# Kernel optimization log

Hardware: AMD Instinct MI355X
Metric: run time of the kernel (lower is better)

## Reference

```python
import jax, jax.numpy as jnp
import numpy as np

NEG_SLOPE = 0.01  # torch.nn.LeakyReLU default


def setup_inputs() -> dict:
    key = jax.random.key(0)
    k1, k2, k3 = jax.random.split(key, 3)
    B, T, U, H, O = 8, 300, 80, 512, 640
    input_TN = jax.random.normal(k1, (B, T, 1, H), dtype=jnp.float32)
    input_PN = jax.random.normal(k2, (B, 1, U, H), dtype=jnp.float32)
    # joint_network: Linear(input_size=2H, n_neurons=O)
    W = jax.random.normal(k3, (2 * H, O), dtype=jnp.float32) / np.sqrt(2 * H)
    b = jnp.zeros((O,), dtype=jnp.float32)
    return {"input_TN": input_TN, "input_PN": input_PN, "W": W, "b": b}


def reference(input_TN, input_PN, W, b):
    # joint == "concat": expand TN/PN to (B,T,U,H), concat on last dim -> (B,T,U,2H),
    # then Linear, then LeakyReLU. Mathematically, Linear(cat(x, y)) ==
    # x @ W[:H] + y @ W[H:] + b, which avoids materializing the (B,T,U,2H) tensor.
    H = input_TN.shape[-1]
    Wt, Wp = W[:H], W[H:]
    tn_proj = jnp.einsum("btuh,ho->btuo", input_TN, Wt)  # (B,T,1,O)
    pn_proj = jnp.einsum("btuh,ho->btuo", input_PN, Wp)  # (B,1,U,O)
    joint = tn_proj + pn_proj + b                         # (B,T,U,O)
    return jax.nn.leaky_relu(joint, negative_slope=NEG_SLOPE)
```

## Files before the change

kernel.cpp:

```cpp
#include <hip/hip_runtime.h>


#define DIM_H 512
#define DIM_O 640
#define DIM_B 8
#define DIM_T 300
#define DIM_U 80
#define M_TN  2400
#define M_PN  640
#define NEG_SLOPE 0.01f

#define BK 32
#define NB_N (DIM_O / 64)
#define NB_TN (((M_TN + 63) / 64) * NB_N)
#define NB_PN (((M_PN + 63) / 64) * NB_N)

typedef float f32x4 __attribute__((ext_vector_type(4)));

__global__ __launch_bounds__(256, 2) void proj_gemm(
    const float* __restrict__ tn_in,
    const float* __restrict__ pn_in,
    const float* __restrict__ W,
    const float* __restrict__ bias,
    float* __restrict__ tn_out,
    float* __restrict__ pn_out)
{
    const int bid = blockIdx.x;
    const float* A; const float* Wp; float* Cout; int M; bool addb; int local;
    if (bid < NB_TN) {
        A = tn_in; Wp = W;                 Cout = tn_out; M = M_TN; addb = false; local = bid;
    } else {
        A = pn_in; Wp = W + DIM_H * DIM_O; Cout = pn_out; M = M_PN; addb = true;  local = bid - NB_TN;
    }
    const int bm = local / NB_N;
    const int bn = local - bm * NB_N;
    const int row0 = bm * 64;
    const int col0 = bn * 64;

    __shared__ float As[BK][68];
    __shared__ float Bs[BK][64];

    const int tid = threadIdx.x;
    const int ty = tid >> 4;
    const int tx = tid & 15;
    const int ar = tid >> 2;
    const int ac = (tid & 3) << 3;
    const int br = tid >> 3;
    const int bc = (tid & 7) << 3;

    float acc[4][4];
    #pragma unroll
    for (int i = 0; i < 4; ++i)
        #pragma unroll
        for (int j = 0; j < 4; ++j) acc[i][j] = 0.f;

    const int gr = row0 + ar;
    const bool arow_ok = (gr < M);
    const float* __restrict__ Arow = A + (size_t)gr * DIM_H;
    const float* __restrict__ Bbase = Wp + col0;

    f32x4 a0 = 0.f, a1 = 0.f, b0, b1;
    if (arow_ok) {
        a0 = *(const f32x4*)(Arow + ac);
        a1 = *(const f32x4*)(Arow + ac + 4);
    }
    b0 = *(const f32x4*)(Bbase + (size_t)br * DIM_O + bc);
    b1 = *(const f32x4*)(Bbase + (size_t)br * DIM_O + bc + 4);

    for (int k0 = 0; k0 < DIM_H; k0 += BK) {
        __syncthreads();
        #pragma unroll
        for (int j = 0; j < 4; ++j) {
            As[ac + j][ar]     = a0[j];
            As[ac + 4 + j][ar] = a1[j];
        }
        *(f32x4*)&Bs[br][bc]     = b0;
        *(f32x4*)&Bs[br][bc + 4] = b1;
        __syncthreads();

        const int kn = k0 + BK;
        if (kn < DIM_H) {
            if (arow_ok) {
                a0 = *(const f32x4*)(Arow + kn + ac);
                a1 = *(const f32x4*)(Arow + kn + ac + 4);
            }
            b0 = *(const f32x4*)(Bbase + (size_t)(kn + br) * DIM_O + bc);
            b1 = *(const f32x4*)(Bbase + (size_t)(kn + br) * DIM_O + bc + 4);
        }

        #pragma unroll
        for (int kk = 0; kk < BK; ++kk) {
            const f32x4 a = *(const f32x4*)&As[kk][ty << 2];
            const f32x4 b = *(const f32x4*)&Bs[kk][tx << 2];
            #pragma unroll
            for (int i = 0; i < 4; ++i) {
                acc[i][0] = fmaf(a[i], b[0], acc[i][0]);
                acc[i][1] = fmaf(a[i], b[1], acc[i][1]);
                acc[i][2] = fmaf(a[i], b[2], acc[i][2]);
                acc[i][3] = fmaf(a[i], b[3], acc[i][3]);
            }
        }
    }

    f32x4 bsv = 0.f;
    if (addb) bsv = *(const f32x4*)(bias + col0 + (tx << 2));
    #pragma unroll
    for (int i = 0; i < 4; ++i) {
        const int r = row0 + (ty << 2) + i;
        if (r < M) {
            f32x4 v;
            #pragma unroll
            for (int j = 0; j < 4; ++j) v[j] = acc[i][j] + bsv[j];
            *(f32x4*)(Cout + (size_t)r * DIM_O + col0 + (tx << 2)) = v;
        }
    }
}

__global__ __launch_bounds__(640) void joint_kernel(
    const float* __restrict__ tn_proj,
    const float* __restrict__ pn_proj,
    float* __restrict__ out)
{
    const int bt = blockIdx.x;
    const int b = bt / DIM_T;
    const int tid = threadIdx.x;

    __shared__ f32x4 tns[DIM_O / 4];
    if (tid < DIM_O / 4)
        tns[tid] = ((const f32x4*)(tn_proj + (size_t)bt * DIM_O))[tid];
    __syncthreads();

    const int o4 = tid % (DIM_O / 4);
    const f32x4 t = tns[o4];

    const f32x4* __restrict__ pn4 = (const f32x4*)(pn_proj + (size_t)b * DIM_U * DIM_O);
    f32x4* __restrict__ out4 = (f32x4*)(out + (size_t)bt * DIM_U * DIM_O);

    #pragma unroll 4
    for (int idx = tid; idx < DIM_U * (DIM_O / 4); idx += 640) {
        const f32x4 p = pn4[idx];
        f32x4 r;
        #pragma unroll
        for (int j = 0; j < 4; ++j) {
            const float x = t[j] + p[j];
            r[j] = fmaxf(x, 0.f) + NEG_SLOPE * fminf(x, 0.f);
        }
        __builtin_nontemporal_store(r, &out4[idx]);
    }
}

extern "C" void kernel_launch(void* const* d_in, const int* in_sizes, int n_in,
                              void* d_out, int out_size, void* d_ws, size_t ws_size,
                              hipStream_t stream) {
    const float* tn   = (const float*)d_in[0];
    const float* pn   = (const float*)d_in[1];
    const float* W    = (const float*)d_in[2];
    const float* bias = (const float*)d_in[3];
    float* out = (float*)d_out;

    float* tn_proj = (float*)d_ws;
    float* pn_proj = tn_proj + (size_t)M_TN * DIM_O;

    proj_gemm<<<NB_TN + NB_PN, 256, 0, stream>>>(tn, pn, W, bias, tn_proj, pn_proj);
    joint_kernel<<<M_TN, 640, 0, stream>>>(tn_proj, pn_proj, out);
}
```

Baseline: 522.6 us.

## Fuse TN projection GEMM with broadcast-add LeakyReLU output epilogue

Splits the work into a small PN projection GEMM and a TN projection GEMM whose epilogue writes the full (B,T,U,O) output directly. It reads pn_proj rows and applies the bias-add and LeakyReLU inside the GEMM. This removes the tn_proj workspace round trip and the separate joint kernel. In exchange, the huge output write is now issued by only 380 blocks of 256 threads, each thread looping over 4 rows × 80 U values. That risks low memory-level parallelism and load imbalance for what is essentially a store-bandwidth-bound kernel.

Result: slower. 539.0 us (+3.1%).

```diff
diff --git a/kernel.cpp b/kernel.cpp
--- a/kernel.cpp
+++ b/kernel.cpp
@@ -3,50 +3,33 @@
 
 #define DIM_H 512
 #define DIM_O 640
-#define DIM_B 8
 #define DIM_T 300
 #define DIM_U 80
 #define M_TN  2400
 #define M_PN  640
 #define NEG_SLOPE 0.01f
-
 #define BK 32
-#define NB_N (DIM_O / 64)
-#define NB_TN (((M_TN + 63) / 64) * NB_N)
-#define NB_PN (((M_PN + 63) / 64) * NB_N)
 
 typedef float f32x4 __attribute__((ext_vector_type(4)));
 
-__global__ __launch_bounds__(256, 2) void proj_gemm(
-    const float* __restrict__ tn_in,
+__global__ __launch_bounds__(256, 2) void pn_gemm(
     const float* __restrict__ pn_in,
     const float* __restrict__ W,
     const float* __restrict__ bias,
-    float* __restrict__ tn_out,
     float* __restrict__ pn_out)
 {
-    const int bid = blockIdx.x;
-    const float* A; const float* Wp; float* Cout; int M; bool addb; int local;
-    if (bid < NB_TN) {
-        A = tn_in; Wp = W;                 Cout = tn_out; M = M_TN; addb = false; local = bid;
-    } else {
-        A = pn_in; Wp = W + DIM_H * DIM_O; Cout = pn_out; M = M_PN; addb = true;  local = bid - NB_TN;
-    }
-    const int bm = local / NB_N;
-    const int bn = local - bm * NB_N;
-    const int row0 = bm * 64;
-    const int col0 = bn * 64;
+    const int bm = blockIdx.x / 10;
+    const int bn = blockIdx.x - bm * 10;
+    const int row0 = bm * 64, col0 = bn * 64;
+    const float* __restrict__ Wp = W + DIM_H * DIM_O;
 
     __shared__ float As[BK][68];
     __shared__ float Bs[BK][64];
 
     const int tid = threadIdx.x;
-    const int ty = tid >> 4;
-    const int tx = tid & 15;
-    const int ar = tid >> 2;
-    const int ac = (tid & 3) << 3;
-    const int br = tid >> 3;
-    const int bc = (tid & 7) << 3;
+    const int ty = tid >> 4, tx = tid & 15;
+    const int ar = tid >> 2, ac = (tid & 3) << 3;
+    const int br = tid >> 3, bc = (tid & 7) << 3;
 
     float acc[4][4];
     #pragma unroll
@@ -54,18 +37,13 @@
         #pragma unroll
         for (int j = 0; j < 4; ++j) acc[i][j] = 0.f;
 
-    const int gr = row0 + ar;
-    const bool arow_ok = (gr < M);
-    const float* __restrict__ Arow = A + (size_t)gr * DIM_H;
+    const float* __restrict__ Arow = pn_in + (size_t)(row0 + ar) * DIM_H;
     const float* __restrict__ Bbase = Wp + col0;
 
-    f32x4 a0 = 0.f, a1 = 0.f, b0, b1;
-    if (arow_ok) {
-        a0 = *(const f32x4*)(Arow + ac);
-        a1 = *(const f32x4*)(Arow + ac + 4);
-    }
-    b0 = *(const f32x4*)(Bbase + (size_t)br * DIM_O + bc);
-    b1 = *(const f32x4*)(Bbase + (size_t)br * DIM_O + bc + 4);
+    f32x4 a0 = *(const f32x4*)(Arow + ac);
+    f32x4 a1 = *(const f32x4*)(Arow + ac + 4);
+    f32x4 b0 = *(const f32x4*)(Bbase + (size_t)br * DIM_O + bc);
+    f32x4 b1 = *(const f32x4*)(Bbase + (size_t)br * DIM_O + bc + 4);
 
     for (int k0 = 0; k0 < DIM_H; k0 += BK) {
         __syncthreads();
@@ -80,10 +58,8 @@
 
         const int kn = k0 + BK;
         if (kn < DIM_H) {
-            if (arow_ok) {
-                a0 = *(const f32x4*)(Arow + kn + ac);
-                a1 = *(const f32x4*)(Arow + kn + ac + 4);
-            }
+            a0 = *(const f32x4*)(Arow + kn + ac);
+            a1 = *(const f32x4*)(Arow + kn + ac + 4);
             b0 = *(const f32x4*)(Bbase + (size_t)(kn + br) * DIM_O + bc);
             b1 = *(const f32x4*)(Bbase + (size_t)(kn + br) * DIM_O + bc + 4);
         }
@@ -102,50 +78,113 @@
         }
     }
 
-    f32x4 bsv = 0.f;
-    if (addb) bsv = *(const f32x4*)(bias + col0 + (tx << 2));
+    const f32x4 bsv = *(const f32x4*)(bias + col0 + (tx << 2));
     #pragma unroll
     for (int i = 0; i < 4; ++i) {
-        const int r = row0 + (ty << 2) + i;
-        if (r < M) {
-            f32x4 v;
-            #pragma unroll
-            for (int j = 0; j < 4; ++j) v[j] = acc[i][j] + bsv[j];
-            *(f32x4*)(Cout + (size_t)r * DIM_O + col0 + (tx << 2)) = v;
-        }
+        f32x4 v;
+        #pragma unroll
+        for (int j = 0; j < 4; ++j) v[j] = acc[i][j] + bsv[j];
+        *(f32x4*)(pn_out + (size_t)(row0 + (ty << 2) + i) * DIM_O + col0 + (tx << 2)) = v;
     }
 }
 
-__global__ __launch_bounds__(640) void joint_kernel(
-    const float* __restrict__ tn_proj,
+__global__ __launch_bounds__(256, 2) void tn_joint(
+    const float* __restrict__ tn_in,
+    const float* __restrict__ W,
     const float* __restrict__ pn_proj,
     float* __restrict__ out)
 {
-    const int bt = blockIdx.x;
-    const int b = bt / DIM_T;
+    const int bm = blockIdx.x / 10;
+    const int bn = blockIdx.x - bm * 10;
+    const int row0 = bm * 64, col0 = bn * 64;
+
+    __shared__ float As[BK][68];
+    __shared__ float Bs[BK][64];
+
     const int tid = threadIdx.x;
-
-    __shared__ f32x4 tns[DIM_O / 4];
-    if (tid < DIM_O / 4)
-        tns[tid] = ((const f32x4*)(tn_proj + (size_t)bt * DIM_O))[tid];
-    __syncthreads();
-
-    const int o4 = tid % (DIM_O / 4);
-    const f32x4 t = tns[o4];
-
-    const f32x4* __restrict__ pn4 = (const f32x4*)(pn_proj + (size_t)b * DIM_U * DIM_O);
-    f32x4* __restrict__ out4 = (f32x4*)(out + (size_t)bt * DIM_U * DIM_O);
-
-    #pragma unroll 4
-    for (int idx = tid; idx < DIM_U * (DIM_O / 4); idx += 640) {
-        const f32x4 p = pn4[idx];
-        f32x4 r;
+    const int ty = tid >> 4, tx = tid & 15;
+    const int ar = tid >> 2, ac = (tid & 3) << 3;
+    const int br = tid >> 3, bc = (tid & 7) << 3;
+
+    float acc[4][4];
+    #pragma unroll
+    for (int i = 0; i < 4; ++i)
+        #pragma unroll
+        for (int j = 0; j < 4; ++j) acc[i][j] = 0.f;
+
+    const int gr = row0 + ar;
+    const bool arow_ok = (gr < M_TN);
+    const float* __restrict__ Arow = tn_in + (size_t)gr * DIM_H;
+    const float* __restrict__ Bbase = W + col0;
+
+    const f32x4 fz = 0.f;
+    f32x4 a0 = fz, a1 = fz, b0, b1;
+    if (arow_ok) {
+        a0 = *(const f32x4*)(Arow + ac);
+        a1 = *(const f32x4*)(Arow + ac + 4);
+    }
+    b0 = *(const f32x4*)(Bbase + (size_t)br * DIM_O + bc);
+    b1 = *(const f32x4*)(Bbase + (size_t)br * DIM_O + bc + 4);
+
+    for (int k0 = 0; k0 < DIM_H; k0 += BK) {
+        __syncthreads();
         #pragma unroll
         for (int j = 0; j < 4; ++j) {
-            const float x = t[j] + p[j];
-            r[j] = fmaxf(x, 0.f) + NEG_SLOPE * fminf(x, 0.f);
-        }
-        __builtin_nontemporal_store(r, &out4[idx]);
+            As[ac + j][ar]     = a0[j];
+            As[ac + 4 + j][ar] = a1[j];
+        }
+        *(f32x4*)&Bs[br][bc]     = b0;
+        *(f32x4*)&Bs[br][bc + 4] = b1;
+        __syncthreads();
+
+        const int kn = k0 + BK;
+        if (kn < DIM_H) {
+            if (arow_ok) {
+                a0 = *(const f32x4*)(Arow + kn + ac);
+                a1 = *(const f32x4*)(Arow + kn + ac + 4);
+            }
+            b0 = *(const f32x4*)(Bbase + (size_t)(kn + br) * DIM_O + bc);
+            b1 = *(const f32x4*)(Bbase + (size_t)(kn + br) * DIM_O + bc + 4);
+        }
+
+        #pragma unroll
+        for (int kk = 0; kk < BK; ++kk) {
+            const f32x4 a = *(const f32x4*)&As[kk][ty << 2];
+            const f32x4 b = *(const f32x4*)&Bs[kk][tx << 2];
+            #pragma unroll
+            for (int i = 0; i < 4; ++i) {
+                acc[i][0] = fmaf(a[i], b[0], acc[i][0]);
+                acc[i][1] = fmaf(a[i], b[1], acc[i][1]);
+                acc[i][2] = fmaf(a[i], b[2], acc[i][2]);
+                acc[i][3] = fmaf(a[i], b[3], acc[i][3]);
+            }
+        }
+    }
+
+    #pragma unroll
+    for (int i = 0; i < 4; ++i) {
+        const int r = row0 + (ty << 2) + i;
+        if (r < M_TN) {
+            const int b = r / DIM_T;
+            f32x4 tv;
+            #pragma unroll
+            for (int j = 0; j < 4; ++j) tv[j] = acc[i][j];
+            const float* __restrict__ pbase =
+                pn_proj + (size_t)b * (DIM_U * DIM_O) + col0 + (tx << 2);
+            float* __restrict__ obase =
+                out + (size_t)r * (DIM_U * DIM_O) + col0 + (tx << 2);
+            #pragma unroll 4
+            for (int u = 0; u < DIM_U; ++u) {
+                const f32x4 p = *(const f32x4*)(pbase + (size_t)u * DIM_O);
+                f32x4 v;
+                #pragma unroll
+                for (int j = 0; j < 4; ++j) {
+                    const float x = tv[j] + p[j];
+                    v[j] = fmaxf(x, 0.f) + NEG_SLOPE * fminf(x, 0.f);
+                }
+                __builtin_nontemporal_store(v, (f32x4*)(obase + (size_t)u * DIM_O));
+            }
+        }
     }
 }
 
@@ -158,9 +197,8 @@
     const float* bias = (const float*)d_in[3];
     float* out = (float*)d_out;
 
-    float* tn_proj = (float*)d_ws;
-    float* pn_proj = tn_proj + (size_t)M_TN * DIM_O;
-
-    proj_gemm<<<NB_TN + NB_PN, 256, 0, stream>>>(tn, pn, W, bias, tn_proj, pn_proj);
-    joint_kernel<<<M_TN, 640, 0, stream>>>(tn_proj, pn_proj, out);
+    float* pn_proj = (float*)d_ws;
+
+    pn_gemm<<<100, 256, 0, stream>>>(pn, W, bias, pn_proj);
+    tn_joint<<<380, 256, 0, stream>>>(tn, W, pn_proj, out);
 }
```
